# Kernel optimization log

Measured on AMD Instinct MI355X. Metric: run time of the kernel, lower is better.

## Reference

```python
import jax, jax.numpy as jnp
import numpy as np

TRAN_DIM = 768
N_HEADS = 8
HEAD_DIM = 96
INNER = N_HEADS * HEAD_DIM  # 768


def setup_inputs() -> dict:
    key = jax.random.key(0)
    k1, k2, k3, k4, k5 = jax.random.split(key, 5)
    x = jax.random.normal(k1, (16, 1024, TRAN_DIM), dtype=jnp.float32)
    s_in = 1.0 / np.sqrt(TRAN_DIM)
    W_qkv = jax.random.uniform(k2, (TRAN_DIM, INNER * 3), jnp.float32, -s_in, s_in)
    b_qkv = jax.random.uniform(k3, (INNER * 3,), jnp.float32, -s_in, s_in)
    s_o = 1.0 / np.sqrt(INNER)
    W_out = jax.random.uniform(k4, (INNER, TRAN_DIM), jnp.float32, -s_o, s_o)
    b_out = jax.random.uniform(k5, (TRAN_DIM,), jnp.float32, -s_o, s_o)
    return {"x": x, "W_qkv": W_qkv, "b_qkv": b_qkv, "W_out": W_out, "b_out": b_out}


def reference(x, W_qkv, b_qkv, W_out, b_out):
    B, N, _ = x.shape
    qkv = x @ W_qkv + b_qkv  # [B, N, 3*INNER]
    q, k, v = jnp.split(qkv, 3, axis=-1)
    # [B, N, INNER] -> [B, H, N, D]
    def to_heads(t):
        return t.reshape(B, N, N_HEADS, HEAD_DIM).transpose(0, 2, 1, 3)
    q, k, v = to_heads(q), to_heads(k), to_heads(v)
    scale = HEAD_DIM ** (-0.5)
    dots = jnp.einsum('bhnd,bhmd->bhnm', q, k) * scale
    attn = jax.nn.softmax(dots, axis=-1)
    out = jnp.einsum('bhnm,bhmd->bhnd', attn, v)
    out = out.transpose(0, 2, 1, 3).reshape(B, N, INNER)
    return out @ W_out + b_out
```

## Files before the change

### kernel.cpp

```cpp
#include <hip/hip_runtime.h>
#include <hip/hip_bf16.h>


#define DEVINL __device__ __forceinline__

typedef __attribute__((ext_vector_type(8))) short s16x8;
typedef __attribute__((ext_vector_type(4))) short s16x4;
typedef __attribute__((ext_vector_type(4))) float f32x4;

DEVINL short f2bf(float f) {
  union { float f; unsigned u; } c; c.f = f;
  unsigned r = c.u + 0x7FFFu + ((c.u >> 16) & 1u);
  return (short)(r >> 16);
}
DEVINL float asf(unsigned u) {
  union { unsigned u; float f; } c; c.u = u; return c.f;
}
DEVINL unsigned pack2(float a, float b) {
  union { float f; unsigned u; } ca, cb; ca.f = a; cb.f = b;
  return (ca.u >> 16) | (cb.u & 0xffff0000u);
}

DEVINL void gload_lds16(const short* g, short* lds) {
  __builtin_amdgcn_global_load_lds((const __attribute__((address_space(1))) void*)g,
                                   (__attribute__((address_space(3))) void*)lds, 16, 0, 0);
}


__global__ void cvt_x_kernel(const float* __restrict__ in, short* __restrict__ out) {
  int i = blockIdx.x * 256 + threadIdx.x;
  float4 v = ((const float4*)in)[i];
  s16x4 o = { f2bf(v.x), f2bf(v.y), f2bf(v.z), f2bf(v.w) };
  *(s16x4*)(out + (size_t)i * 4) = o;
}

__global__ void tcvt_kernel(const float* __restrict__ in, short* __restrict__ out, int R, int C) {
  __shared__ float t[32][33];
  int tx = threadIdx.x & 31, ty = threadIdx.x >> 5;
  int r0 = blockIdx.y * 32, c0 = blockIdx.x * 32;
#pragma unroll
  for (int i = 0; i < 4; i++) {
    int r = ty + i * 8;
    t[r][tx] = in[(size_t)(r0 + r) * C + c0 + tx];
  }
  __syncthreads();
#pragma unroll
  for (int i = 0; i < 4; i++) {
    int r = ty + i * 8;
    out[(size_t)(c0 + r) * R + r0 + tx] = f2bf(t[tx][r]);
  }
}

__global__ void vtrans_kernel(const short* __restrict__ qkvb, short* __restrict__ out) {
  __shared__ short t[32][34];
  int tx = threadIdx.x & 31, ty = threadIdx.x >> 5;
  int d0 = blockIdx.x * 32, n0 = blockIdx.y * 32;
  int pair = blockIdx.z;
  int b = pair >> 3, h = pair & 7;
#pragma unroll
  for (int i = 0; i < 4; i++) {
    int r = ty + i * 8;
    t[r][tx] = qkvb[(size_t)(b * 1024 + n0 + r) * 2304 + 1536 + h * 96 + d0 + tx];
  }
  __syncthreads();
  size_t obase = (size_t)pair * 96 * 1024;
#pragma unroll
  for (int i = 0; i < 4; i++) {
    int r = ty + i * 8;
    out[obase + (size_t)(d0 + r) * 1024 + n0 + tx] = t[tx][r];
  }
}


template <int MODE>
__global__ __launch_bounds__(512, 2) void gemm256(const short* __restrict__ A, const short* __restrict__ Bt,
                                                  const float* __restrict__ bias, int K, int nTn,
                                                  short* __restrict__ qkvb, float* __restrict__ outf) {
  __shared__ short lds[65536];
  short* const ldsA = lds;
  short* const ldsB = lds + 32768;
  const int tid = threadIdx.x;
  const int l = tid & 63, w = tid >> 6;
  const int lo = l & 15, hi = l >> 4;
  const int wm = w >> 2, wn = w & 3;

  int cpx = gridDim.x >> 3;
  int bid = blockIdx.x;
  int swz = (bid & 7) * cpx + (bid >> 3);
  int tm = swz / nTn, tn = swz - tm * nTn;

  const int NKT = K >> 6;
  const int NIT = NKT >> 1;

  const int rS = tid >> 3;
  const int ko = (((tid & 7) ^ (rS & 7)) << 3);
  const short* aS = A + (size_t)(tm * 256 + rS) * K + ko;
  const short* bS = Bt + (size_t)(tn * 256 + ((rS >> 5) << 6) + (rS & 31)) * K + ko;
  const size_t step128 = (size_t)128 * K;

  f32x4 acc[8][4] = {};

#define STAGE_A(kt, q, buf) do {                                        \
    const short* s_ = aS + (size_t)(q) * 64 * K + (kt) * 64;            \
    short* d_ = ldsA + ((buf) * 2 + (q)) * 8192 + tid * 8;              \
    gload_lds16(s_, d_); gload_lds16(s_ + step128, d_ + 4096); } while (0)
#define STAGE_B(kt, q, buf) do {                                        \
    const short* s_ = bS + (size_t)(q) * 32 * K + (kt) * 64;            \
    short* d_ = ldsB + ((buf) * 2 + (q)) * 8192 + tid * 8;              \
    gload_lds16(s_, d_); gload_lds16(s_ + step128, d_ + 4096); } while (0)

#define DS_A(AF, bufc, qm) do {                                                   \
    const short* p_ = ldsA + ((bufc) * 2 + (qm)) * 8192 + (wm * 64 + lo) * 64;    \
    _Pragma("unroll") for (int mi = 0; mi < 4; mi++)                              \
      _Pragma("unroll") for (int kk = 0; kk < 2; kk++)                            \
        AF[mi][kk] = *(const s16x8*)(p_ + mi * 1024 + (((kk * 4 + hi) ^ (lo & 7)) << 3)); } while (0)
#define DS_B(BF, bufc, qn) do {                                                   \
    const short* p_ = ldsB + ((bufc) * 2 + (qn)) * 8192 + (wn * 32 + lo) * 64;    \
    _Pragma("unroll") for (int ni = 0; ni < 2; ni++)                              \
      _Pragma("unroll") for (int kk = 0; kk < 2; kk++)                            \
        BF[ni][kk] = *(const s16x8*)(p_ + ni * 1024 + (((kk * 4 + hi) ^ (lo & 7)) << 3)); } while (0)

#define BAR() do { __builtin_amdgcn_sched_barrier(0); __builtin_amdgcn_s_barrier(); \
                   __builtin_amdgcn_sched_barrier(0); } while (0)
#define MFMA16(qm, qn, AF, BF) do {                                               \
    __builtin_amdgcn_s_setprio(1);                                                \
    _Pragma("unroll") for (int kk = 0; kk < 2; kk++)                              \
      _Pragma("unroll") for (int mi = 0; mi < 4; mi++)                            \
        _Pragma("unroll") for (int ni = 0; ni < 2; ni++)                          \
          acc[(qm) * 4 + mi][(qn) * 2 + ni] = __builtin_amdgcn_mfma_f32_16x16x32_bf16( \
              AF[mi][kk], BF[ni][kk], acc[(qm) * 4 + mi][(qn) * 2 + ni], 0, 0, 0); \
    __builtin_amdgcn_s_setprio(0);                                                \
    __builtin_amdgcn_sched_barrier(0); } while (0)

  STAGE_A(0, 0, 0); STAGE_B(0, 0, 0);
  STAGE_A(0, 1, 0); STAGE_B(0, 1, 0);
  STAGE_A(1, 0, 1); STAGE_B(1, 0, 1);
  asm volatile("s_waitcnt vmcnt(4)" ::: "memory");
  __builtin_amdgcn_s_barrier();

  s16x8 af[4][2], bfa[2][2], bfb[2][2];
#pragma unroll 1
  for (int i = 0; i < NIT; i++) {
    int T = 2 * i;
    bool last = (i == NIT - 1);
    DS_A(af, 0, 0); DS_B(bfa, 0, 0);
    if (T + 1 < NKT) STAGE_A(T + 1, 1, 1);
    BAR(); MFMA16(0, 0, af, bfa); BAR();
    DS_B(bfb, 0, 1);
    if (T + 1 < NKT) STAGE_B(T + 1, 1, 1);
    BAR(); MFMA16(0, 1, af, bfb); BAR();
    DS_A(af, 0, 1);
    if (T + 2 < NKT) STAGE_A(T + 2, 0, 0);
    BAR(); MFMA16(1, 0, af, bfa); BAR();
    if (T + 2 < NKT) STAGE_B(T + 2, 0, 0);
    BAR(); MFMA16(1, 1, af, bfb);
    if (last) { asm volatile("s_waitcnt vmcnt(0)" ::: "memory"); }
    else      { asm volatile("s_waitcnt vmcnt(4)" ::: "memory"); }
    BAR();
    DS_A(af, 1, 0); DS_B(bfa, 1, 0);
    if (T + 2 < NKT) STAGE_A(T + 2, 1, 0);
    BAR(); MFMA16(0, 0, af, bfa); BAR();
    DS_B(bfb, 1, 1);
    if (T + 2 < NKT) STAGE_B(T + 2, 1, 0);
    BAR(); MFMA16(0, 1, af, bfb); BAR();
    DS_A(af, 1, 1);
    if (T + 3 < NKT) STAGE_A(T + 3, 0, 1);
    BAR(); MFMA16(1, 0, af, bfa); BAR();
    if (T + 3 < NKT) STAGE_B(T + 3, 0, 1);
    BAR(); MFMA16(1, 1, af, bfb);
    if (!last) { asm volatile("s_waitcnt vmcnt(4)" ::: "memory"); }
    BAR();
  }
#undef STAGE_A
#undef STAGE_B
#undef DS_A
#undef DS_B
#undef BAR
#undef MFMA16

  if (MODE == 0) {
    const float qscale = 0.14724444757204526f;
#pragma unroll
    for (int ni = 0; ni < 4; ni++) {
      int colr = wn * 64 + ni * 16 + lo;
      int coln = tn * 256 + colr;
      float bv = bias[coln];
      float scl = (coln < 768) ? qscale : 1.0f;
#pragma unroll
      for (int mi = 0; mi < 8; mi++)
#pragma unroll
        for (int j = 0; j < 4; j++) {
          int rowr = wm * 128 + mi * 16 + hi * 4 + j;
          lds[rowr * 256 + colr] = f2bf((acc[mi][ni][j] + bv) * scl);
        }
    }
    __syncthreads();
    short* dstb = qkvb + (size_t)(tm * 256) * 2304 + tn * 256;
#pragma unroll
    for (int k = 0; k < 16; k++) {
      int g = k * 512 + tid;
      int r = g >> 5, c = g & 31;
      *(s16x8*)(dstb + (size_t)r * 2304 + c * 8) = *(const s16x8*)(lds + r * 256 + c * 8);
    }
  } else {
#pragma unroll
    for (int ni = 0; ni < 4; ni++) {
      int coln = tn * 256 + wn * 64 + ni * 16 + lo;
      float bv = bias[coln];
#pragma unroll
      for (int mi = 0; mi < 8; mi++) {
#pragma unroll
        for (int j = 0; j < 4; j++) {
          int rowm = tm * 256 + wm * 128 + mi * 16 + hi * 4 + j;
          outf[(size_t)rowm * 768 + coln] = acc[mi][ni][j] + bv;
        }
      }
    }
  }
}


__global__ __launch_bounds__(512) void attn_kernel(const short* __restrict__ qkvb,
                                                   const short* __restrict__ vtb,
                                                   short* __restrict__ attn_out) {
  __shared__ short Klds[64 * 104];
  __shared__ short Vlds[96 * 64];
  int tid = threadIdx.x, lane = tid & 63, wid = tid >> 6;
  int lo = lane & 15, hi = lane >> 4;
  int bid = blockIdx.x;
  int pair = bid & 127, qt = bid >> 7;
  int b = pair >> 3, h = pair & 7;
  const short* Vtp = vtb + (size_t)pair * 1024 * 96;
  int qrow0 = qt * 128 + wid * 16;

  s16x8 qf[3];
#pragma unroll
  for (int dk = 0; dk < 3; dk++)
    qf[dk] = *(const s16x8*)(qkvb + (size_t)(b * 1024 + qrow0 + lo) * 2304 +
                             h * 96 + dk * 32 + hi * 8);

  const short* sp[3];
  short* sdst[3];
  size_t sstep[3];
#pragma unroll
  for (int i = 0; i < 3; i++) {
    int c = i * 512 + tid;
    if (c < 768) {
      int krow = c / 12, kcc = c - krow * 12;
      sdst[i] = Klds + krow * 104 + kcc * 8;
      sp[i] = qkvb + (size_t)(b * 1024 + krow) * 2304 + 768 + h * 96 + kcc * 8;
      sstep[i] = (size_t)64 * 2304;
    } else {
      int d = c - 768;
      int vrow = d >> 3, vcc = d & 7;
      sdst[i] = Vlds + vrow * 64 + ((vcc ^ (vrow & 7)) * 8);
      sp[i] = Vtp + (size_t)vrow * 1024 + vcc * 8;
      sstep[i] = 64;
    }
  }

  f32x4 accO[6] = {};
  float lsum = 0.0f;

  s16x8 sreg[3];
#pragma unroll
  for (int i = 0; i < 3; i++) sreg[i] = *(const s16x8*)sp[i];

  for (int t = 0; t < 16; t++) {
    __syncthreads();
#pragma unroll
    for (int i = 0; i < 3; i++) *(s16x8*)sdst[i] = sreg[i];
    __syncthreads();

    int t2 = (t + 1) & 15;
#pragma unroll
    for (int i = 0; i < 3; i++)
      sreg[i] = *(const s16x8*)(sp[i] + (size_t)t2 * sstep[i]);

    f32x4 st[4] = {};
#pragma unroll
    for (int kb2 = 0; kb2 < 4; kb2++) {
#pragma unroll
      for (int dk = 0; dk < 3; dk++) {
        s16x8 kf = *(const s16x8*)(Klds + (kb2 * 16 + lo) * 104 + dk * 32 + hi * 8);
        st[kb2] = __builtin_amdgcn_mfma_f32_16x16x32_bf16(kf, qf[dk], st[kb2], 0, 0, 0);
      }
    }

    unsigned u[4][2];
#pragma unroll
    for (int kb2 = 0; kb2 < 4; kb2++) {
      float p0 = __builtin_amdgcn_exp2f(st[kb2][0]);
      float p1 = __builtin_amdgcn_exp2f(st[kb2][1]);
      float p2 = __builtin_amdgcn_exp2f(st[kb2][2]);
      float p3 = __builtin_amdgcn_exp2f(st[kb2][3]);
      unsigned w0 = pack2(p0, p1);
      unsigned w1 = pack2(p2, p3);
      u[kb2][0] = w0;
      u[kb2][1] = w1;
      lsum += (asf(w0 << 16) + asf(w0 & 0xffff0000u)) +
              (asf(w1 << 16) + asf(w1 & 0xffff0000u));
    }

    int s0 = ((lane >> 4) & 1) * 32 + lo;
    int s1 = s0 + 16;
    bool hiSel = (lane & 32) != 0;
#pragma unroll
    for (int c2 = 0; c2 < 2; c2++) {
      union { unsigned w[4]; s16x8 v; } pa;
      {
        unsigned a0 = (unsigned)__shfl((int)u[2 * c2][0], s0, 64);
        unsigned b0 = (unsigned)__shfl((int)u[2 * c2 + 1][0], s0, 64);
        unsigned a1 = (unsigned)__shfl((int)u[2 * c2][1], s0, 64);
        unsigned b1 = (unsigned)__shfl((int)u[2 * c2 + 1][1], s0, 64);
        unsigned a2 = (unsigned)__shfl((int)u[2 * c2][0], s1, 64);
        unsigned b2 = (unsigned)__shfl((int)u[2 * c2 + 1][0], s1, 64);
        unsigned a3 = (unsigned)__shfl((int)u[2 * c2][1], s1, 64);
        unsigned b3 = (unsigned)__shfl((int)u[2 * c2 + 1][1], s1, 64);
        pa.w[0] = hiSel ? b0 : a0;
        pa.w[1] = hiSel ? b1 : a1;
        pa.w[2] = hiSel ? b2 : a2;
        pa.w[3] = hiSel ? b3 : a3;
      }
#pragma unroll
      for (int db = 0; db < 6; db++) {
        int d = db * 16 + lo;
        s16x8 vf = *(const s16x8*)(Vlds + d * 64 + (((c2 * 4 + hi) ^ (d & 7)) * 8));
        accO[db] = __builtin_amdgcn_mfma_f32_16x16x32_bf16(pa.v, vf, accO[db], 0, 0, 0);
      }
    }
  }

  float s = lsum;
  s += __shfl_xor(s, 16, 64);
  s += __shfl_xor(s, 32, 64);
  float r = 1.0f / s;
  float rj[4];
#pragma unroll
  for (int j = 0; j < 4; j++)
    rj[j] = __shfl(r, hi * 4 + j, 64);

#pragma unroll
  for (int db = 0; db < 6; db++)
#pragma unroll
    for (int j = 0; j < 4; j++) {
      int qrow = qrow0 + hi * 4 + j;
      int d = db * 16 + lo;
      attn_out[((size_t)b * 1024 + qrow) * 768 + h * 96 + d] = f2bf(accO[db][j] * rj[j]);
    }
}


extern "C" void kernel_launch(void* const* d_in, const int* in_sizes, int n_in,
                              void* d_out, int out_size, void* d_ws, size_t ws_size,
                              hipStream_t stream) {
  const float* x = (const float*)d_in[0];
  const float* Wqkv = (const float*)d_in[1];
  const float* bqkv = (const float*)d_in[2];
  const float* Wout = (const float*)d_in[3];
  const float* bout = (const float*)d_in[4];
  float* out = (float*)d_out;

  char* ws = (char*)d_ws;
  short* xb = (short*)ws;
  short* wqkvT = (short*)(ws + 25165824);
  short* woutT = (short*)(ws + 28704768);
  short* qkvb = (short*)(ws + 29884416);
  short* vtb = (short*)(ws + 105381888);

  cvt_x_kernel<<<12288, 256, 0, stream>>>(x, xb);
  tcvt_kernel<<<dim3(72, 24), 256, 0, stream>>>(Wqkv, wqkvT, 768, 2304);
  tcvt_kernel<<<dim3(24, 24), 256, 0, stream>>>(Wout, woutT, 768, 768);

  gemm256<0><<<576, 512, 0, stream>>>(xb, wqkvT, bqkv, 768, 9, qkvb, nullptr);
  vtrans_kernel<<<dim3(3, 32, 128), 256, 0, stream>>>(qkvb, vtb);
  attn_kernel<<<1024, 512, 0, stream>>>(qkvb, vtb, xb);
  gemm256<1><<<192, 512, 0, stream>>>(xb, woutT, bout, 768, 3, nullptr, out);
}
```

Before: 222.2 us.

## Switch attention to 32x32x16 MFMA with 32-row warps and swizzled K tiles

Rewrites the attention kernel to use 32x32x16 bf16 MFMA instead of 16x16x32. Each wave now handles 32 query rows, and blocks shrink from 512 to 256 threads. K is split into two XOR-swizzled LDS tiles with a row permutation (swap23), so the S accumulator layout feeds directly into the P·V MFMA without cross-lane shuffles. This is meant to remove shuffle overhead and reduce LDS traffic per FLOP, at the cost of more registers per thread and fewer threads to stage each tile.

```diff
diff --git a/kernel.cpp b/kernel.cpp
--- a/kernel.cpp
+++ b/kernel.cpp
@@ -7,6 +7,7 @@
 typedef __attribute__((ext_vector_type(8))) short s16x8;
 typedef __attribute__((ext_vector_type(4))) short s16x4;
 typedef __attribute__((ext_vector_type(4))) float f32x4;
+typedef __attribute__((ext_vector_type(16))) float f32x16;
 
 DEVINL short f2bf(float f) {
   union { float f; unsigned u; } c; c.f = f;
@@ -20,6 +21,7 @@
   union { float f; unsigned u; } ca, cb; ca.f = a; cb.f = b;
   return (ca.u >> 16) | (cb.u & 0xffff0000u);
 }
+DEVINL int swap23(int k) { return (k & ~12) | ((k & 4) << 1) | ((k & 8) >> 1); }
 
 DEVINL void gload_lds16(const short* g, short* lds) {
   __builtin_amdgcn_global_load_lds((const __attribute__((address_space(1))) void*)g,
@@ -220,133 +222,119 @@
 }
 
 
-__global__ __launch_bounds__(512) void attn_kernel(const short* __restrict__ qkvb,
+__global__ __launch_bounds__(256) void attn_kernel(const short* __restrict__ qkvb,
                                                    const short* __restrict__ vtb,
                                                    short* __restrict__ attn_out) {
-  __shared__ short Klds[64 * 104];
+  __shared__ short Ka[64 * 64];
+  __shared__ short Kb[64 * 32];
   __shared__ short Vlds[96 * 64];
   int tid = threadIdx.x, lane = tid & 63, wid = tid >> 6;
-  int lo = lane & 15, hi = lane >> 4;
+  int q31 = lane & 31, hi2 = lane >> 5;
   int bid = blockIdx.x;
   int pair = bid & 127, qt = bid >> 7;
   int b = pair >> 3, h = pair & 7;
   const short* Vtp = vtb + (size_t)pair * 1024 * 96;
-  int qrow0 = qt * 128 + wid * 16;
-
-  s16x8 qf[3];
-#pragma unroll
-  for (int dk = 0; dk < 3; dk++)
-    qf[dk] = *(const s16x8*)(qkvb + (size_t)(b * 1024 + qrow0 + lo) * 2304 +
-                             h * 96 + dk * 32 + hi * 8);
-
-  const short* sp[3];
-  short* sdst[3];
-  size_t sstep[3];
-#pragma unroll
-  for (int i = 0; i < 3; i++) {
-    int c = i * 512 + tid;
-    if (c < 768) {
+  int qrow0 = qt * 128 + wid * 32;
+
+  s16x8 qf[6];
+#pragma unroll
+  for (int dc = 0; dc < 6; dc++)
+    qf[dc] = *(const s16x8*)(qkvb + (size_t)(b * 1024 + qrow0 + q31) * 2304 +
+                             h * 96 + dc * 16 + hi2 * 8);
+
+  const short* sp[6];
+  short* sdst[6];
+  int sstep[6];
+#pragma unroll
+  for (int i = 0; i < 6; i++) {
+    if (i < 3) {
+      int c = i * 256 + tid;
       int krow = c / 12, kcc = c - krow * 12;
-      sdst[i] = Klds + krow * 104 + kcc * 8;
+      int lam = swap23(krow);
+      sdst[i] = (kcc < 8) ? Ka + lam * 64 + ((kcc ^ (lam & 7)) << 3)
+                          : Kb + lam * 32 + (((kcc - 8) ^ (lam & 3)) << 3);
       sp[i] = qkvb + (size_t)(b * 1024 + krow) * 2304 + 768 + h * 96 + kcc * 8;
-      sstep[i] = (size_t)64 * 2304;
+      sstep[i] = 64 * 2304;
     } else {
-      int d = c - 768;
+      int d = (i - 3) * 256 + tid;
       int vrow = d >> 3, vcc = d & 7;
-      sdst[i] = Vlds + vrow * 64 + ((vcc ^ (vrow & 7)) * 8);
+      sdst[i] = Vlds + vrow * 64 + ((vcc ^ (vrow & 7)) << 3);
       sp[i] = Vtp + (size_t)vrow * 1024 + vcc * 8;
       sstep[i] = 64;
     }
   }
 
-  f32x4 accO[6] = {};
+  f32x16 accO[3] = {};
   float lsum = 0.0f;
 
-  s16x8 sreg[3];
-#pragma unroll
-  for (int i = 0; i < 3; i++) sreg[i] = *(const s16x8*)sp[i];
+  s16x8 sreg[6];
+#pragma unroll
+  for (int i = 0; i < 6; i++) sreg[i] = *(const s16x8*)sp[i];
 
   for (int t = 0; t < 16; t++) {
     __syncthreads();
 #pragma unroll
-    for (int i = 0; i < 3; i++) *(s16x8*)sdst[i] = sreg[i];
+    for (int i = 0; i < 6; i++) *(s16x8*)sdst[i] = sreg[i];
     __syncthreads();
 
     int t2 = (t + 1) & 15;
 #pragma unroll
-    for (int i = 0; i < 3; i++)
+    for (int i = 0; i < 6; i++)
       sreg[i] = *(const s16x8*)(sp[i] + (size_t)t2 * sstep[i]);
 
-    f32x4 st[4] = {};
-#pragma unroll
-    for (int kb2 = 0; kb2 < 4; kb2++) {
-#pragma unroll
-      for (int dk = 0; dk < 3; dk++) {
-        s16x8 kf = *(const s16x8*)(Klds + (kb2 * 16 + lo) * 104 + dk * 32 + hi * 8);
-        st[kb2] = __builtin_amdgcn_mfma_f32_16x16x32_bf16(kf, qf[dk], st[kb2], 0, 0, 0);
+#pragma unroll
+    for (int kb = 0; kb < 2; kb++) {
+      f32x16 st = {};
+#pragma unroll
+      for (int dc = 0; dc < 6; dc++) {
+        int c = dc * 2 + hi2;
+        int lam = kb * 32 + q31;
+        const short* kp = (c < 8) ? Ka + lam * 64 + ((c ^ (lam & 7)) << 3)
+                                  : Kb + lam * 32 + (((c - 8) ^ (lam & 3)) << 3);
+        s16x8 kf = *(const s16x8*)kp;
+        st = __builtin_amdgcn_mfma_f32_32x32x16_bf16(kf, qf[dc], st, 0, 0, 0);
       }
-    }
-
-    unsigned u[4][2];
-#pragma unroll
-    for (int kb2 = 0; kb2 < 4; kb2++) {
-      float p0 = __builtin_amdgcn_exp2f(st[kb2][0]);
-      float p1 = __builtin_amdgcn_exp2f(st[kb2][1]);
-      float p2 = __builtin_amdgcn_exp2f(st[kb2][2]);
-      float p3 = __builtin_amdgcn_exp2f(st[kb2][3]);
-      unsigned w0 = pack2(p0, p1);
-      unsigned w1 = pack2(p2, p3);
-      u[kb2][0] = w0;
-      u[kb2][1] = w1;
-      lsum += (asf(w0 << 16) + asf(w0 & 0xffff0000u)) +
-              (asf(w1 << 16) + asf(w1 & 0xffff0000u));
-    }
-
-    int s0 = ((lane >> 4) & 1) * 32 + lo;
-    int s1 = s0 + 16;
-    bool hiSel = (lane & 32) != 0;
-#pragma unroll
-    for (int c2 = 0; c2 < 2; c2++) {
-      union { unsigned w[4]; s16x8 v; } pa;
-      {
-        unsigned a0 = (unsigned)__shfl((int)u[2 * c2][0], s0, 64);
-        unsigned b0 = (unsigned)__shfl((int)u[2 * c2 + 1][0], s0, 64);
-        unsigned a1 = (unsigned)__shfl((int)u[2 * c2][1], s0, 64);
-        unsigned b1 = (unsigned)__shfl((int)u[2 * c2 + 1][1], s0, 64);
-        unsigned a2 = (unsigned)__shfl((int)u[2 * c2][0], s1, 64);
-        unsigned b2 = (unsigned)__shfl((int)u[2 * c2 + 1][0], s1, 64);
-        unsigned a3 = (unsigned)__shfl((int)u[2 * c2][1], s1, 64);
-        unsigned b3 = (unsigned)__shfl((int)u[2 * c2 + 1][1], s1, 64);
-        pa.w[0] = hiSel ? b0 : a0;
-        pa.w[1] = hiSel ? b1 : a1;
-        pa.w[2] = hiSel ? b2 : a2;
-        pa.w[3] = hiSel ? b3 : a3;
+
+      unsigned u[8];
+#pragma unroll
+      for (int i = 0; i < 8; i++) {
+        float p0 = __builtin_amdgcn_exp2f(st[2 * i]);
+        float p1 = __builtin_amdgcn_exp2f(st[2 * i + 1]);
+        unsigned w = pack2(p0, p1);
+        u[i] = w;
+        lsum += asf(w << 16) + asf(w & 0xffff0000u);
       }
-#pragma unroll
-      for (int db = 0; db < 6; db++) {
-        int d = db * 16 + lo;
-        s16x8 vf = *(const s16x8*)(Vlds + d * 64 + (((c2 * 4 + hi) ^ (d & 7)) * 8));
-        accO[db] = __builtin_amdgcn_mfma_f32_16x16x32_bf16(pa.v, vf, accO[db], 0, 0, 0);
+
+#pragma unroll
+      for (int half = 0; half < 2; half++) {
+        union { unsigned w[4]; s16x8 v; } pa;
+#pragma unroll
+        for (int wi = 0; wi < 4; wi++) pa.w[wi] = u[half * 4 + wi];
+        int kc = kb * 2 + half;
+#pragma unroll
+        for (int db = 0; db < 3; db++) {
+          int d = db * 32 + q31;
+          s16x8 vf = *(const s16x8*)(Vlds + d * 64 + (((kc * 2 + hi2) ^ (d & 7)) << 3));
+          accO[db] = __builtin_amdgcn_mfma_f32_32x32x16_bf16(pa.v, vf, accO[db], 0, 0, 0);
+        }
       }
     }
   }
 
-  float s = lsum;
-  s += __shfl_xor(s, 16, 64);
-  s += __shfl_xor(s, 32, 64);
-  float r = 1.0f / s;
-  float rj[4];
-#pragma unroll
-  for (int j = 0; j < 4; j++)
-    rj[j] = __shfl(r, hi * 4 + j, 64);
-
-#pragma unroll
-  for (int db = 0; db < 6; db++)
-#pragma unroll
-    for (int j = 0; j < 4; j++) {
-      int qrow = qrow0 + hi * 4 + j;
-      int d = db * 16 + lo;
-      attn_out[((size_t)b * 1024 + qrow) * 768 + h * 96 + d] = f2bf(accO[db][j] * rj[j]);
+  float s = lsum + __shfl_xor(lsum, 32, 64);
+  float rinv = 1.0f / s;
+  float rr[16];
+#pragma unroll
+  for (int r = 0; r < 16; r++)
+    rr[r] = __shfl(rinv, (r & 3) + 8 * (r >> 2) + 4 * hi2, 64);
+
+#pragma unroll
+  for (int db = 0; db < 3; db++)
+#pragma unroll
+    for (int r = 0; r < 16; r++) {
+      int qrow = qrow0 + (r & 3) + 8 * (r >> 2) + 4 * hi2;
+      int d = db * 32 + q31;
+      attn_out[((size_t)b * 1024 + qrow) * 768 + h * 96 + d] = f2bf(accO[db][r] * rr[r]);
     }
 }
 
@@ -374,6 +362,6 @@
 
   gemm256<0><<<576, 512, 0, stream>>>(xb, wqkvT, bqkv, 768, 9, qkvb, nullptr);
   vtrans_kernel<<<dim3(3, 32, 128), 256, 0, stream>>>(qkvb, vtb);
-  attn_kernel<<<1024, 512, 0, stream>>>(qkvb, vtb, xb);
+  attn_kernel<<<1024, 256, 0, stream>>>(qkvb, vtb, xb);
   gemm256<1><<<192, 512, 0, stream>>>(xb, woutT, bout, 768, 3, nullptr, out);
 }
```

Result: faster. 208.4 us (-6.2%).
